# Performance work log

Measured on AMD Instinct MI355X. Metric: run time of the kernel, lower is better.

The kernel has to match this reference:

```python
import jax, jax.numpy as jnp
import numpy as np

NEG_INF = -1e9


def setup_inputs() -> dict:
    key = jax.random.key(0)
    k1, k2, k3, k4 = jax.random.split(key, 4)
    B, S, D, P = 4, 256, 512, 256
    sequence = jax.random.normal(k1, (B, S, D), dtype=jnp.float32)
    sequence_mask = jnp.ones((B, S), dtype=jnp.float32)
    W1 = jax.random.normal(k2, (P, D), dtype=jnp.float32) * (1.0 / np.sqrt(D))
    W2 = jax.random.normal(k3, (P, D), dtype=jnp.float32) * (1.0 / np.sqrt(D))
    v = jax.random.normal(k4, (P,), dtype=jnp.float32) * (1.0 / np.sqrt(P))
    return {"sequence": sequence, "sequence_mask": sequence_mask,
            "W1": W1, "W2": W2, "v": v}


def reference(sequence, sequence_mask, W1, W2, v):
    # sequence: [B, S, D]; sequence_mask: [B, S] (1 = valid)
    # Projection (additive) self-attention, vectorized over all query positions.
    pk = jnp.einsum('bsd,pd->bsp', sequence, W1)  # key projections  [B, S, P]
    pq = jnp.einsum('bsd,pd->bsp', sequence, W2)  # query projections [B, S, P]
    # scores[b, i, j] = v . tanh(pq[b, i] + pk[b, j])   (i = query, j = key)
    scores = jnp.einsum('bijp,p->bij',
                        jnp.tanh(pq[:, :, None, :] + pk[:, None, :, :]), v)
    # mask keys, softmax over key dim
    key_mask = sequence_mask[:, None, :] > 0          # [B, 1, S]
    scores = jnp.where(key_mask, scores, NEG_INF)
    weights = jax.nn.softmax(scores, axis=-1)         # [B, Sq, Sk]
    attn = jnp.einsum('bij,bjd->bid', weights, sequence)  # [B, S, D]
    # mask_sequence: zero out invalid query positions
    attn = attn * sequence_mask[:, :, None]
    weights = weights * sequence_mask[:, :, None]
    return attn, weights
```

## Files before the change

kernel.cpp:

```cpp
#include <hip/hip_runtime.h>

constexpr int B = 4;
constexpr int S = 256;
constexpr int D = 512;
constexpr int P = 256;
constexpr float NEG_INF = -1e9f;
constexpr float LOG2E = 1.4426950408889634f;
constexpr float C2 = 2.885390081777927f;

__device__ __forceinline__ float fast_exp2(float x) {
#if __has_builtin(__builtin_amdgcn_exp2f)
    return __builtin_amdgcn_exp2f(x);
#else
    return exp2f(x);
#endif
}

__device__ __forceinline__ float fast_rcp(float x) {
#if __has_builtin(__builtin_amdgcn_rcpf)
    return __builtin_amdgcn_rcpf(x);
#else
    return 1.0f / x;
#endif
}

__global__ __launch_bounds__(256)
void proj_kernel(const float* __restrict__ seq,
                 const float* __restrict__ W1, const float* __restrict__ W2,
                 float* __restrict__ Eq, float* __restrict__ EkT) {
    __shared__ float As[64][34];
    __shared__ float Ws[64][68];

    int bid0 = blockIdx.x;
    int bid = (bid0 & 7) * 32 + (bid0 >> 3);

    const float* A;
    const float* Bp;
    float* out;
    if (bid < 128) {
        int mt = bid >> 2, nt = bid & 3;
        A = seq + (size_t)mt * 32 * D;
        Bp = W2 + (size_t)nt * 64 * D;
        out = Eq + (size_t)mt * 32 * 256 + nt * 64;
    } else {
        int r = bid - 128;
        int b = r >> 5, t = r & 31;
        int mt = t >> 2, nt = t & 3;
        A = W1 + (size_t)mt * 32 * D;
        Bp = seq + ((size_t)b * S + nt * 64) * D;
        out = EkT + (size_t)b * P * S + (size_t)mt * 32 * 256 + nt * 64;
    }

    int tid = threadIdx.x;
    int tx = tid & 15, ty = tid >> 4;
    int ar = tid >> 3, acg = tid & 7;
    int br = tid >> 2, bcg = tid & 3;
    const float* aptr = A + (size_t)ar * D + acg * 8;
    const float* bptr = Bp + (size_t)br * D + bcg * 16;

    float4 a0, a1, w0, w1, w2, w3;
    a0 = *(const float4*)(aptr);      a1 = *(const float4*)(aptr + 4);
    w0 = *(const float4*)(bptr);      w1 = *(const float4*)(bptr + 4);
    w2 = *(const float4*)(bptr + 8);  w3 = *(const float4*)(bptr + 12);

    float c0[4] = {0.f, 0.f, 0.f, 0.f};
    float c1[4] = {0.f, 0.f, 0.f, 0.f};

    for (int kt = 0; kt < 8; kt++) {
        int ka = acg * 8;
        As[ka + 0][ar] = a0.x; As[ka + 1][ar] = a0.y;
        As[ka + 2][ar] = a0.z; As[ka + 3][ar] = a0.w;
        As[ka + 4][ar] = a1.x; As[ka + 5][ar] = a1.y;
        As[ka + 6][ar] = a1.z; As[ka + 7][ar] = a1.w;
        int kb = bcg * 16;
        Ws[kb + 0][br] = w0.x;  Ws[kb + 1][br] = w0.y;
        Ws[kb + 2][br] = w0.z;  Ws[kb + 3][br] = w0.w;
        Ws[kb + 4][br] = w1.x;  Ws[kb + 5][br] = w1.y;
        Ws[kb + 6][br] = w1.z;  Ws[kb + 7][br] = w1.w;
        Ws[kb + 8][br] = w2.x;  Ws[kb + 9][br] = w2.y;
        Ws[kb + 10][br] = w2.z; Ws[kb + 11][br] = w2.w;
        Ws[kb + 12][br] = w3.x; Ws[kb + 13][br] = w3.y;
        Ws[kb + 14][br] = w3.z; Ws[kb + 15][br] = w3.w;
        __syncthreads();
        if (kt < 7) {
            const float* ap = aptr + (kt + 1) * 64;
            const float* bp = bptr + (kt + 1) * 64;
            a0 = *(const float4*)(ap);     a1 = *(const float4*)(ap + 4);
            w0 = *(const float4*)(bp);     w1 = *(const float4*)(bp + 4);
            w2 = *(const float4*)(bp + 8); w3 = *(const float4*)(bp + 12);
        }
#pragma unroll 8
        for (int k = 0; k < 64; k++) {
            float2 av = *(const float2*)&As[k][ty * 2];
            float4 wv = *(const float4*)&Ws[k][tx * 4];
            c0[0] = fmaf(av.x, wv.x, c0[0]);
            c0[1] = fmaf(av.x, wv.y, c0[1]);
            c0[2] = fmaf(av.x, wv.z, c0[2]);
            c0[3] = fmaf(av.x, wv.w, c0[3]);
            c1[0] = fmaf(av.y, wv.x, c1[0]);
            c1[1] = fmaf(av.y, wv.y, c1[1]);
            c1[2] = fmaf(av.y, wv.z, c1[2]);
            c1[3] = fmaf(av.y, wv.w, c1[3]);
        }
        __syncthreads();
    }
    float4 o0 = {fast_exp2(c0[0] * C2), fast_exp2(c0[1] * C2),
                 fast_exp2(c0[2] * C2), fast_exp2(c0[3] * C2)};
    float4 o1 = {fast_exp2(c1[0] * C2), fast_exp2(c1[1] * C2),
                 fast_exp2(c1[2] * C2), fast_exp2(c1[3] * C2)};
    *(float4*)&out[(size_t)(ty * 2 + 0) * 256 + tx * 4] = o0;
    *(float4*)&out[(size_t)(ty * 2 + 1) * 256 + tx * 4] = o1;
}

__global__ __launch_bounds__(512)
void score_attn_kernel(const float* __restrict__ seq,
                       const float* __restrict__ EkT, const float* __restrict__ Eq,
                       const float* __restrict__ v, const float* __restrict__ mask,
                       float* __restrict__ wout, float* __restrict__ attn) {
    __shared__ float Eqs[4][P];
    __shared__ float vsm[P];
    __shared__ float ekb[2][32][256];
    __shared__ float part[2][4][S];
    __shared__ float wsm[S][4];
    __shared__ float p3[4][4][D];
    __shared__ float redm[4][8], reds[4][8];

    int bid0 = blockIdx.x;
    int bid = (bid0 & 7) * 32 + (bid0 >> 3);
    int b = bid >> 6;
    int i0 = (bid & 63) * 4;
    int tid = threadIdx.x;
    int lane = tid & 63, wid = tid >> 6;

    const float* ekbase = EkT + (size_t)b * P * S;

    float4 r0, r1, r2, r3;
#define LOADC(c)                                                       \
    {                                                                  \
        const float4* sp_ = (const float4*)(ekbase + (c) * 8192);      \
        r0 = sp_[tid]; r1 = sp_[tid + 512];                            \
        r2 = sp_[tid + 1024]; r3 = sp_[tid + 1536];                    \
    }
#define WRITEC(bf)                                                     \
    {                                                                  \
        float4* dp_ = (float4*)&ekb[bf][0][0];                         \
        dp_[tid] = r0; dp_[tid + 512] = r1;                            \
        dp_[tid + 1024] = r2; dp_[tid + 1536] = r3;                    \
    }

    LOADC(0);
    ((float2*)Eqs)[tid] = ((const float2*)(Eq + ((size_t)b * S + i0) * P))[tid];
    if (tid < 128) {
        float2 vv = ((const float2*)v)[tid];
        ((float2*)vsm)[tid] = make_float2(-2.f * vv.x, -2.f * vv.y);
    }
    WRITEC(0);
    LOADC(1);
    __syncthreads();

    int j = tid & 255, h = tid >> 8;
    float acc[4] = {0.f, 0.f, 0.f, 0.f};
    for (int c = 0; c < 8; c++) {
        int cur = c & 1;
        int pl0 = h * 16;
        int pg0 = c * 32 + pl0;
#pragma unroll
        for (int t = 0; t < 4; t++) {
            int pl = pl0 + t * 4, pg = pg0 + t * 4;
            float e0 = ekb[cur][pl + 0][j];
            float e1 = ekb[cur][pl + 1][j];
            float e2 = ekb[cur][pl + 2][j];
            float e3 = ekb[cur][pl + 3][j];
            float4 vv = *(const float4*)&vsm[pg];
#pragma unroll
            for (int q = 0; q < 4; q++) {
                float4 eq = *(const float4*)&Eqs[q][pg];
                acc[q] = fmaf(vv.x, fast_rcp(fmaf(e0, eq.x, 1.f)), acc[q]);
                acc[q] = fmaf(vv.y, fast_rcp(fmaf(e1, eq.y, 1.f)), acc[q]);
                acc[q] = fmaf(vv.z, fast_rcp(fmaf(e2, eq.z, 1.f)), acc[q]);
                acc[q] = fmaf(vv.w, fast_rcp(fmaf(e3, eq.w, 1.f)), acc[q]);
            }
        }
        if (c < 7) { WRITEC(cur ^ 1); }
        if (c < 6) { LOADC(c + 2); }
        __syncthreads();
    }
#undef LOADC
#undef WRITEC
#pragma unroll
    for (int q = 0; q < 4; q++) part[h][q][j] = acc[q];
    __syncthreads();

    float s[4], e[4] = {0.f, 0.f, 0.f, 0.f};
    if (tid < 256) {
        float km = mask[(size_t)b * S + j];
#pragma unroll
        for (int q = 0; q < 4; q++) {
            float sv = part[0][q][j] + part[1][q][j];
            s[q] = (km > 0.f) ? sv : NEG_INF;
            float mm = s[q];
#pragma unroll
            for (int off = 32; off >= 1; off >>= 1)
                mm = fmaxf(mm, __shfl_xor(mm, off, 64));
            if (lane == 0) redm[q][wid] = mm;
        }
    }
    __syncthreads();
    if (tid < 256) {
#pragma unroll
        for (int q = 0; q < 4; q++) {
            float mm = fmaxf(fmaxf(redm[q][0], redm[q][1]),
                             fmaxf(redm[q][2], redm[q][3]));
            float ee = fast_exp2((s[q] - mm) * LOG2E);
            e[q] = ee;
            float ss = ee;
#pragma unroll
            for (int off = 32; off >= 1; off >>= 1)
                ss += __shfl_xor(ss, off, 64);
            if (lane == 0) reds[q][wid] = ss;
        }
    }
    __syncthreads();
    if (tid < 256) {
#pragma unroll
        for (int q = 0; q < 4; q++) {
            float ssum = (reds[q][0] + reds[q][1]) + (reds[q][2] + reds[q][3]);
            float qm = mask[(size_t)b * S + i0 + q];
            float w = e[q] * fast_rcp(ssum) * qm;
            wsm[j][q] = w;
            wout[((size_t)b * S + i0 + q) * S + j] = w;
        }
    }
    __syncthreads();

    {
        int dg = tid & 127, jh = tid >> 7;
        int d0 = dg * 4;
        const float4* sp = (const float4*)(seq + (size_t)b * S * D);
        float4 A0 = {0.f, 0.f, 0.f, 0.f}, A1 = {0.f, 0.f, 0.f, 0.f};
        float4 A2 = {0.f, 0.f, 0.f, 0.f}, A3 = {0.f, 0.f, 0.f, 0.f};
#pragma unroll 4
        for (int jj = 0; jj < 64; jj++) {
            int jx = jh * 64 + jj;
            float4 s4 = sp[(size_t)jx * 128 + dg];
            float4 w4 = *(const float4*)&wsm[jx][0];
            A0.x = fmaf(w4.x, s4.x, A0.x); A0.y = fmaf(w4.x, s4.y, A0.y);
            A0.z = fmaf(w4.x, s4.z, A0.z); A0.w = fmaf(w4.x, s4.w, A0.w);
            A1.x = fmaf(w4.y, s4.x, A1.x); A1.y = fmaf(w4.y, s4.y, A1.y);
            A1.z = fmaf(w4.y, s4.z, A1.z); A1.w = fmaf(w4.y, s4.w, A1.w);
            A2.x = fmaf(w4.z, s4.x, A2.x); A2.y = fmaf(w4.z, s4.y, A2.y);
            A2.z = fmaf(w4.z, s4.z, A2.z); A2.w = fmaf(w4.z, s4.w, A2.w);
            A3.x = fmaf(w4.w, s4.x, A3.x); A3.y = fmaf(w4.w, s4.y, A3.y);
            A3.z = fmaf(w4.w, s4.z, A3.z); A3.w = fmaf(w4.w, s4.w, A3.w);
        }
        *(float4*)&p3[jh][0][d0] = A0;
        *(float4*)&p3[jh][1][d0] = A1;
        *(float4*)&p3[jh][2][d0] = A2;
        *(float4*)&p3[jh][3][d0] = A3;
    }
    __syncthreads();
    {
        int d = tid;
#pragma unroll
        for (int q = 0; q < 4; q++) {
            float r = (p3[0][q][d] + p3[1][q][d]) + (p3[2][q][d] + p3[3][q][d]);
            attn[((size_t)b * S + i0 + q) * D + d] = r;
        }
    }
}

extern "C" void kernel_launch(void* const* d_in, const int* in_sizes, int n_in,
                              void* d_out, int out_size, void* d_ws, size_t ws_size,
                              hipStream_t stream) {
    const float* seq  = (const float*)d_in[0];
    const float* mask = (const float*)d_in[1];
    const float* W1   = (const float*)d_in[2];
    const float* W2   = (const float*)d_in[3];
    const float* v    = (const float*)d_in[4];

    float* attn = (float*)d_out;
    float* wout = attn + (size_t)B * S * D;

    float* Eq  = (float*)d_ws;
    float* EkT = Eq + (size_t)B * S * P;

    proj_kernel<<<256, 256, 0, stream>>>(seq, W1, W2, Eq, EkT);
    score_attn_kernel<<<B * (S / 4), 512, 0, stream>>>(seq, EkT, Eq, v, mask,
                                                       wout, attn);
}
```

Before: 41.29 us.

## Split attention GEMM into separate kernel and shrink projection tiles

Splits the fused score+attention kernel into a score/softmax kernel and a standalone tiled GEMM kernel that reads the weights back from the output buffer to compute attn. The projection kernel now uses 16-row tiles with 512 blocks instead of 32-row tiles with 256 blocks, giving more parallelism. The score kernel drops its double-buffered EkT staging for a simpler single buffer with two syncs per chunk. This trades register and shared-memory pressure and better occupancy against an extra launch, a global round trip of the weights, and lost load/compute overlap.

```diff
diff --git a/kernel.cpp b/kernel.cpp
--- a/kernel.cpp
+++ b/kernel.cpp
@@ -28,101 +28,88 @@
 void proj_kernel(const float* __restrict__ seq,
                  const float* __restrict__ W1, const float* __restrict__ W2,
                  float* __restrict__ Eq, float* __restrict__ EkT) {
-    __shared__ float As[64][34];
+    __shared__ float As[64][17];
     __shared__ float Ws[64][68];
 
     int bid0 = blockIdx.x;
-    int bid = (bid0 & 7) * 32 + (bid0 >> 3);
+    int bid = (bid0 & 7) * 64 + (bid0 >> 3);
 
     const float* A;
     const float* Bp;
     float* out;
-    if (bid < 128) {
+    if (bid < 256) {
         int mt = bid >> 2, nt = bid & 3;
-        A = seq + (size_t)mt * 32 * D;
+        A = seq + (size_t)mt * 16 * D;
         Bp = W2 + (size_t)nt * 64 * D;
-        out = Eq + (size_t)mt * 32 * 256 + nt * 64;
+        out = Eq + (size_t)mt * 16 * 256 + nt * 64;
     } else {
-        int r = bid - 128;
-        int b = r >> 5, t = r & 31;
+        int r = bid - 256;
+        int b = r >> 6, t = r & 63;
         int mt = t >> 2, nt = t & 3;
-        A = W1 + (size_t)mt * 32 * D;
+        A = W1 + (size_t)mt * 16 * D;
         Bp = seq + ((size_t)b * S + nt * 64) * D;
-        out = EkT + (size_t)b * P * S + (size_t)mt * 32 * 256 + nt * 64;
+        out = EkT + (size_t)b * P * S + (size_t)mt * 16 * 256 + nt * 64;
     }
 
     int tid = threadIdx.x;
     int tx = tid & 15, ty = tid >> 4;
-    int ar = tid >> 3, acg = tid & 7;
-    int br = tid >> 2, bcg = tid & 3;
-    const float* aptr = A + (size_t)ar * D + acg * 8;
-    const float* bptr = Bp + (size_t)br * D + bcg * 16;
-
-    float4 a0, a1, w0, w1, w2, w3;
-    a0 = *(const float4*)(aptr);      a1 = *(const float4*)(aptr + 4);
+    int arow = tid >> 4, akc = tid & 15;
+    int brow = tid >> 2, bcg = tid & 3;
+    const float* aptr = A + (size_t)arow * D + akc * 4;
+    const float* bptr = Bp + (size_t)brow * D + bcg * 16;
+
+    float4 a0, w0, w1, w2, w3;
+    a0 = *(const float4*)(aptr);
     w0 = *(const float4*)(bptr);      w1 = *(const float4*)(bptr + 4);
     w2 = *(const float4*)(bptr + 8);  w3 = *(const float4*)(bptr + 12);
 
     float c0[4] = {0.f, 0.f, 0.f, 0.f};
-    float c1[4] = {0.f, 0.f, 0.f, 0.f};
 
     for (int kt = 0; kt < 8; kt++) {
-        int ka = acg * 8;
-        As[ka + 0][ar] = a0.x; As[ka + 1][ar] = a0.y;
-        As[ka + 2][ar] = a0.z; As[ka + 3][ar] = a0.w;
-        As[ka + 4][ar] = a1.x; As[ka + 5][ar] = a1.y;
-        As[ka + 6][ar] = a1.z; As[ka + 7][ar] = a1.w;
+        int ka = akc * 4;
+        As[ka + 0][arow] = a0.x; As[ka + 1][arow] = a0.y;
+        As[ka + 2][arow] = a0.z; As[ka + 3][arow] = a0.w;
         int kb = bcg * 16;
-        Ws[kb + 0][br] = w0.x;  Ws[kb + 1][br] = w0.y;
-        Ws[kb + 2][br] = w0.z;  Ws[kb + 3][br] = w0.w;
-        Ws[kb + 4][br] = w1.x;  Ws[kb + 5][br] = w1.y;
-        Ws[kb + 6][br] = w1.z;  Ws[kb + 7][br] = w1.w;
-        Ws[kb + 8][br] = w2.x;  Ws[kb + 9][br] = w2.y;
-        Ws[kb + 10][br] = w2.z; Ws[kb + 11][br] = w2.w;
-        Ws[kb + 12][br] = w3.x; Ws[kb + 13][br] = w3.y;
-        Ws[kb + 14][br] = w3.z; Ws[kb + 15][br] = w3.w;
+        Ws[kb + 0][brow] = w0.x;  Ws[kb + 1][brow] = w0.y;
+        Ws[kb + 2][brow] = w0.z;  Ws[kb + 3][brow] = w0.w;
+        Ws[kb + 4][brow] = w1.x;  Ws[kb + 5][brow] = w1.y;
+        Ws[kb + 6][brow] = w1.z;  Ws[kb + 7][brow] = w1.w;
+        Ws[kb + 8][brow] = w2.x;  Ws[kb + 9][brow] = w2.y;
+        Ws[kb + 10][brow] = w2.z; Ws[kb + 11][brow] = w2.w;
+        Ws[kb + 12][brow] = w3.x; Ws[kb + 13][brow] = w3.y;
+        Ws[kb + 14][brow] = w3.z; Ws[kb + 15][brow] = w3.w;
         __syncthreads();
         if (kt < 7) {
             const float* ap = aptr + (kt + 1) * 64;
             const float* bp = bptr + (kt + 1) * 64;
-            a0 = *(const float4*)(ap);     a1 = *(const float4*)(ap + 4);
+            a0 = *(const float4*)(ap);
             w0 = *(const float4*)(bp);     w1 = *(const float4*)(bp + 4);
             w2 = *(const float4*)(bp + 8); w3 = *(const float4*)(bp + 12);
         }
 #pragma unroll 8
         for (int k = 0; k < 64; k++) {
-            float2 av = *(const float2*)&As[k][ty * 2];
+            float av = As[k][ty];
             float4 wv = *(const float4*)&Ws[k][tx * 4];
-            c0[0] = fmaf(av.x, wv.x, c0[0]);
-            c0[1] = fmaf(av.x, wv.y, c0[1]);
-            c0[2] = fmaf(av.x, wv.z, c0[2]);
-            c0[3] = fmaf(av.x, wv.w, c0[3]);
-            c1[0] = fmaf(av.y, wv.x, c1[0]);
-            c1[1] = fmaf(av.y, wv.y, c1[1]);
-            c1[2] = fmaf(av.y, wv.z, c1[2]);
-            c1[3] = fmaf(av.y, wv.w, c1[3]);
+            c0[0] = fmaf(av, wv.x, c0[0]);
+            c0[1] = fmaf(av, wv.y, c0[1]);
+            c0[2] = fmaf(av, wv.z, c0[2]);
+            c0[3] = fmaf(av, wv.w, c0[3]);
         }
         __syncthreads();
     }
     float4 o0 = {fast_exp2(c0[0] * C2), fast_exp2(c0[1] * C2),
                  fast_exp2(c0[2] * C2), fast_exp2(c0[3] * C2)};
-    float4 o1 = {fast_exp2(c1[0] * C2), fast_exp2(c1[1] * C2),
-                 fast_exp2(c1[2] * C2), fast_exp2(c1[3] * C2)};
-    *(float4*)&out[(size_t)(ty * 2 + 0) * 256 + tx * 4] = o0;
-    *(float4*)&out[(size_t)(ty * 2 + 1) * 256 + tx * 4] = o1;
+    *(float4*)&out[(size_t)ty * 256 + tx * 4] = o0;
 }
 
 __global__ __launch_bounds__(512)
-void score_attn_kernel(const float* __restrict__ seq,
-                       const float* __restrict__ EkT, const float* __restrict__ Eq,
-                       const float* __restrict__ v, const float* __restrict__ mask,
-                       float* __restrict__ wout, float* __restrict__ attn) {
+void score_kernel(const float* __restrict__ EkT, const float* __restrict__ Eq,
+                  const float* __restrict__ v, const float* __restrict__ mask,
+                  float* __restrict__ wout) {
     __shared__ float Eqs[4][P];
     __shared__ float vsm[P];
-    __shared__ float ekb[2][32][256];
+    __shared__ float ekb[16][256];
     __shared__ float part[2][4][S];
-    __shared__ float wsm[S][4];
-    __shared__ float p3[4][4][D];
     __shared__ float redm[4][8], reds[4][8];
 
     int bid0 = blockIdx.x;
@@ -134,43 +121,30 @@
 
     const float* ekbase = EkT + (size_t)b * P * S;
 
-    float4 r0, r1, r2, r3;
-#define LOADC(c)                                                       \
-    {                                                                  \
-        const float4* sp_ = (const float4*)(ekbase + (c) * 8192);      \
-        r0 = sp_[tid]; r1 = sp_[tid + 512];                            \
-        r2 = sp_[tid + 1024]; r3 = sp_[tid + 1536];                    \
-    }
-#define WRITEC(bf)                                                     \
-    {                                                                  \
-        float4* dp_ = (float4*)&ekb[bf][0][0];                         \
-        dp_[tid] = r0; dp_[tid + 512] = r1;                            \
-        dp_[tid + 1024] = r2; dp_[tid + 1536] = r3;                    \
-    }
-
-    LOADC(0);
     ((float2*)Eqs)[tid] = ((const float2*)(Eq + ((size_t)b * S + i0) * P))[tid];
     if (tid < 128) {
         float2 vv = ((const float2*)v)[tid];
         ((float2*)vsm)[tid] = make_float2(-2.f * vv.x, -2.f * vv.y);
     }
-    WRITEC(0);
-    LOADC(1);
-    __syncthreads();
 
     int j = tid & 255, h = tid >> 8;
     float acc[4] = {0.f, 0.f, 0.f, 0.f};
-    for (int c = 0; c < 8; c++) {
-        int cur = c & 1;
-        int pl0 = h * 16;
-        int pg0 = c * 32 + pl0;
-#pragma unroll
-        for (int t = 0; t < 4; t++) {
-            int pl = pl0 + t * 4, pg = pg0 + t * 4;
-            float e0 = ekb[cur][pl + 0][j];
-            float e1 = ekb[cur][pl + 1][j];
-            float e2 = ekb[cur][pl + 2][j];
-            float e3 = ekb[cur][pl + 3][j];
+    for (int c = 0; c < 16; c++) {
+        {
+            const float4* src = (const float4*)(ekbase + (size_t)c * 4096);
+            float4* dp = (float4*)&ekb[0][0];
+            dp[tid] = src[tid];
+            dp[tid + 512] = src[tid + 512];
+        }
+        __syncthreads();
+#pragma unroll
+        for (int t = 0; t < 2; t++) {
+            int pl = h * 8 + t * 4;
+            int pg = c * 16 + pl;
+            float e0 = ekb[pl + 0][j];
+            float e1 = ekb[pl + 1][j];
+            float e2 = ekb[pl + 2][j];
+            float e3 = ekb[pl + 3][j];
             float4 vv = *(const float4*)&vsm[pg];
 #pragma unroll
             for (int q = 0; q < 4; q++) {
@@ -181,12 +155,8 @@
                 acc[q] = fmaf(vv.w, fast_rcp(fmaf(e3, eq.w, 1.f)), acc[q]);
             }
         }
-        if (c < 7) { WRITEC(cur ^ 1); }
-        if (c < 6) { LOADC(c + 2); }
-        __syncthreads();
-    }
-#undef LOADC
-#undef WRITEC
+        __syncthreads();
+    }
 #pragma unroll
     for (int q = 0; q < 4; q++) part[h][q][j] = acc[q];
     __syncthreads();
@@ -227,46 +197,68 @@
             float ssum = (reds[q][0] + reds[q][1]) + (reds[q][2] + reds[q][3]);
             float qm = mask[(size_t)b * S + i0 + q];
             float w = e[q] * fast_rcp(ssum) * qm;
-            wsm[j][q] = w;
             wout[((size_t)b * S + i0 + q) * S + j] = w;
         }
     }
-    __syncthreads();
-
-    {
-        int dg = tid & 127, jh = tid >> 7;
-        int d0 = dg * 4;
-        const float4* sp = (const float4*)(seq + (size_t)b * S * D);
-        float4 A0 = {0.f, 0.f, 0.f, 0.f}, A1 = {0.f, 0.f, 0.f, 0.f};
-        float4 A2 = {0.f, 0.f, 0.f, 0.f}, A3 = {0.f, 0.f, 0.f, 0.f};
-#pragma unroll 4
-        for (int jj = 0; jj < 64; jj++) {
-            int jx = jh * 64 + jj;
-            float4 s4 = sp[(size_t)jx * 128 + dg];
-            float4 w4 = *(const float4*)&wsm[jx][0];
-            A0.x = fmaf(w4.x, s4.x, A0.x); A0.y = fmaf(w4.x, s4.y, A0.y);
-            A0.z = fmaf(w4.x, s4.z, A0.z); A0.w = fmaf(w4.x, s4.w, A0.w);
-            A1.x = fmaf(w4.y, s4.x, A1.x); A1.y = fmaf(w4.y, s4.y, A1.y);
-            A1.z = fmaf(w4.y, s4.z, A1.z); A1.w = fmaf(w4.y, s4.w, A1.w);
-            A2.x = fmaf(w4.z, s4.x, A2.x); A2.y = fmaf(w4.z, s4.y, A2.y);
-            A2.z = fmaf(w4.z, s4.z, A2.z); A2.w = fmaf(w4.z, s4.w, A2.w);
-            A3.x = fmaf(w4.w, s4.x, A3.x); A3.y = fmaf(w4.w, s4.y, A3.y);
-            A3.z = fmaf(w4.w, s4.z, A3.z); A3.w = fmaf(w4.w, s4.w, A3.w);
-        }
-        *(float4*)&p3[jh][0][d0] = A0;
-        *(float4*)&p3[jh][1][d0] = A1;
-        *(float4*)&p3[jh][2][d0] = A2;
-        *(float4*)&p3[jh][3][d0] = A3;
-    }
-    __syncthreads();
-    {
-        int d = tid;
-#pragma unroll
-        for (int q = 0; q < 4; q++) {
-            float r = (p3[0][q][d] + p3[1][q][d]) + (p3[2][q][d] + p3[3][q][d]);
-            attn[((size_t)b * S + i0 + q) * D + d] = r;
-        }
-    }
+}
+
+__global__ __launch_bounds__(256)
+void attn_kernel(const float* __restrict__ wts, const float* __restrict__ seq,
+                 float* __restrict__ attn) {
+    __shared__ float As[64][17];
+    __shared__ float Ws[64][68];
+
+    int bid0 = blockIdx.x;
+    int bid = (bid0 & 7) * 64 + (bid0 >> 3);
+    int b = bid >> 7;
+    int t = bid & 127;
+    int i0 = (t >> 3) * 16;
+    int d0 = (t & 7) * 64;
+
+    int tid = threadIdx.x;
+    int tx = tid & 15, ty = tid >> 4;
+    int arow = tid >> 4, akc = tid & 15;
+    int brow = tid >> 2, bcg = tid & 3;
+    const float* aptr = wts + ((size_t)b * S + i0 + arow) * S + akc * 4;
+    const float* bptr = seq + ((size_t)b * S + brow) * D + d0 + bcg * 16;
+
+    float4 a0, w0, w1, w2, w3;
+    a0 = *(const float4*)(aptr);
+    w0 = *(const float4*)(bptr);      w1 = *(const float4*)(bptr + 4);
+    w2 = *(const float4*)(bptr + 8);  w3 = *(const float4*)(bptr + 12);
+
+    float c0[4] = {0.f, 0.f, 0.f, 0.f};
+
+    for (int kt = 0; kt < 4; kt++) {
+        int ka = akc * 4;
+        As[ka + 0][arow] = a0.x; As[ka + 1][arow] = a0.y;
+        As[ka + 2][arow] = a0.z; As[ka + 3][arow] = a0.w;
+        int kb = bcg * 16;
+        *(float4*)&Ws[brow][kb + 0] = w0;
+        *(float4*)&Ws[brow][kb + 4] = w1;
+        *(float4*)&Ws[brow][kb + 8] = w2;
+        *(float4*)&Ws[brow][kb + 12] = w3;
+        __syncthreads();
+        if (kt < 3) {
+            const float* ap = aptr + (kt + 1) * 64;
+            const float* bp = bptr + (size_t)(kt + 1) * 64 * D;
+            a0 = *(const float4*)(ap);
+            w0 = *(const float4*)(bp);     w1 = *(const float4*)(bp + 4);
+            w2 = *(const float4*)(bp + 8); w3 = *(const float4*)(bp + 12);
+        }
+#pragma unroll 8
+        for (int k = 0; k < 64; k++) {
+            float av = As[k][ty];
+            float4 wv = *(const float4*)&Ws[k][tx * 4];
+            c0[0] = fmaf(av, wv.x, c0[0]);
+            c0[1] = fmaf(av, wv.y, c0[1]);
+            c0[2] = fmaf(av, wv.z, c0[2]);
+            c0[3] = fmaf(av, wv.w, c0[3]);
+        }
+        __syncthreads();
+    }
+    *(float4*)&attn[((size_t)b * S + i0 + ty) * D + d0 + tx * 4] =
+        make_float4(c0[0], c0[1], c0[2], c0[3]);
 }
 
 extern "C" void kernel_launch(void* const* d_in, const int* in_sizes, int n_in,
@@ -284,7 +276,7 @@
     float* Eq  = (float*)d_ws;
     float* EkT = Eq + (size_t)B * S * P;
 
-    proj_kernel<<<256, 256, 0, stream>>>(seq, W1, W2, Eq, EkT);
-    score_attn_kernel<<<B * (S / 4), 512, 0, stream>>>(seq, EkT, Eq, v, mask,
-                                                       wout, attn);
-}
+    proj_kernel<<<512, 256, 0, stream>>>(seq, W1, W2, Eq, EkT);
+    score_kernel<<<B * (S / 4), 512, 0, stream>>>(EkT, Eq, v, mask, wout);
+    attn_kernel<<<512, 256, 0, stream>>>(wout, seq, attn);
+}
```

New measurement: 59.97 us. 1.45x slower.
